# Optimization experiments

Measured on AMD Instinct MI355X. Metric: run time of the kernel, lower is better.

## Reference

```python
import jax, jax.numpy as jnp
import numpy as np

H = 32          # hidden_size
NUM_LAYERS = 3
B, T, IN = 16384, 64, 2


def _gru_dir(x, Wih, Whh, bih, bhh, reverse):
    """Single-direction GRU over x:[B,T,I] with PyTorch gate math."""
    # Precompute input projections for all timesteps: [B,T,3H]
    xg = jnp.einsum('bti,gi->btg', x, Wih) + bih
    if reverse:
        xg = xg[:, ::-1]

    def step(h, xt):
        gh = h @ Whh.T + bhh                      # [B,3H]
        xr, xz, xn = jnp.split(xt, 3, axis=-1)
        hr, hz, hn = jnp.split(gh, 3, axis=-1)
        r = jax.nn.sigmoid(xr + hr)
        z = jax.nn.sigmoid(xz + hz)
        n = jnp.tanh(xn + r * hn)
        h2 = (1.0 - z) * n + z * h
        return h2, h2

    h0 = jnp.zeros((x.shape[0], H), x.dtype)
    _, hs = jax.lax.scan(step, h0, jnp.swapaxes(xg, 0, 1))  # [T,B,H]
    hs = jnp.swapaxes(hs, 0, 1)                              # [B,T,H]
    if reverse:
        hs = hs[:, ::-1]
    return hs


def setup_inputs() -> dict:
    key = jax.random.key(0)
    ks = jax.random.split(key, 11)
    s = 0.2  # weight scale ~ uniform(-1/sqrt(H)) magnitude
    return {
        'x':    jax.random.normal(ks[0], (B, T, IN), jnp.float32),
        'Wih0': jax.random.normal(ks[1], (2, 3 * H, IN), jnp.float32) * s,
        'Whh0': jax.random.normal(ks[2], (2, 3 * H, H), jnp.float32) * s,
        'bih0': jax.random.normal(ks[3], (2, 3 * H), jnp.float32) * s,
        'bhh0': jax.random.normal(ks[4], (2, 3 * H), jnp.float32) * s,
        'Wih':  jax.random.normal(ks[5], (NUM_LAYERS - 1, 2, 3 * H, 2 * H), jnp.float32) * s,
        'Whh':  jax.random.normal(ks[6], (NUM_LAYERS - 1, 2, 3 * H, H), jnp.float32) * s,
        'bih':  jax.random.normal(ks[7], (NUM_LAYERS - 1, 2, 3 * H), jnp.float32) * s,
        'bhh':  jax.random.normal(ks[8], (NUM_LAYERS - 1, 2, 3 * H), jnp.float32) * s,
        'Wfc':  jax.random.normal(ks[9], (2, 2 * H), jnp.float32) * s,
        'bfc':  jax.random.normal(ks[10], (2,), jnp.float32) * s,
    }


def reference(x, Wih0, Whh0, bih0, bhh0, Wih, Whh, bih, bhh, Wfc, bfc):
    out = x
    for l in range(NUM_LAYERS):
        if l == 0:
            wi, wh, bi, bh = Wih0, Whh0, bih0, bhh0
        else:
            wi, wh, bi, bh = Wih[l - 1], Whh[l - 1], bih[l - 1], bhh[l - 1]
        fwd = _gru_dir(out, wi[0], wh[0], bi[0], bh[0], reverse=False)
        bwd = _gru_dir(out, wi[1], wh[1], bi[1], bh[1], reverse=True)
        out = jnp.concatenate([fwd, bwd], axis=-1)  # [B,T,2H]
    y = out @ Wfc.T + bfc                            # [B,T,2]
    return jnp.tanh(y)
```

## Files before the change

kernel.cpp:

```cpp
#include <hip/hip_runtime.h>
#include <cstdint>
#include <cstddef>


#define BB 16384
#define TT 64
#define ST ((size_t)BB * 64)
#define PT ((size_t)TT * BB * 2)

typedef __attribute__((ext_vector_type(8))) _Float16 f16x8;
typedef __attribute__((ext_vector_type(4))) float f32x4;

#if __has_builtin(__builtin_amdgcn_exp2f)
#define EXP2(x) __builtin_amdgcn_exp2f(x)
#else
#define EXP2(x) exp2f(x)
#endif
#if __has_builtin(__builtin_amdgcn_rcpf)
#define RCP(x) __builtin_amdgcn_rcpf(x)
#else
#define RCP(x) (1.0f / (x))
#endif

#define SR (-1.4426950408889634f)
#define SN (-2.8853900817779268f)

__device__ __forceinline__ float tanh_fast(float x) { return 2.0f / (1.0f + __expf(-2.0f * x)) - 1.0f; }
__device__ __forceinline__ unsigned short f2h(float f) {
    _Float16 h = (_Float16)f;
    return __builtin_bit_cast(unsigned short, h);
}
__device__ __forceinline__ unsigned int cvt_pkh(float a, float b) {
#if __has_builtin(__builtin_amdgcn_cvt_pkrtz)
    typedef __fp16 h2_t __attribute__((ext_vector_type(2)));
    h2_t p = __builtin_amdgcn_cvt_pkrtz(a, b);
    return __builtin_bit_cast(unsigned int, p);
#else
    return (unsigned int)f2h(a) | ((unsigned int)f2h(b) << 16);
#endif
}
__device__ __forceinline__ f32x4 mfma16h(f16x8 a, f16x8 b, f32x4 c) {
    return __builtin_amdgcn_mfma_f32_16x16x32_f16(a, b, c, 0, 0, 0);
}

__device__ __forceinline__ void gate_pair(float aR0, float aR1, float aZ0, float aZ1,
                                          float xN0, float xN1, float hN0, float hN1,
                                          float& hp0, float& hp1) {
    float er0 = EXP2(aR0), er1 = EXP2(aR1);
    float ez0 = EXP2(aZ0), ez1 = EXP2(aZ1);
    float Ar0 = 1.f + er0, Ar1 = 1.f + er1;
    float Az0 = 1.f + ez0, Az1 = 1.f + ez1;
    float iR = RCP(Ar0 * Ar1);
    float iZ = RCP(Az0 * Az1);
    float r0 = iR * Ar1, r1 = iR * Ar0;
    float z0 = iZ * Az1, z1 = iZ * Az0;
    float v0 = fmaf(r0, hN0, xN0), v1 = fmaf(r1, hN1, xN1);
    float en0 = EXP2(v0), en1 = EXP2(v1);
    float An0 = 1.f + en0, An1 = 1.f + en1;
    float iN = RCP(An0 * An1);
    float n0 = fmaf(2.f, iN * An1, -1.f);
    float n1 = fmaf(2.f, iN * An0, -1.f);
    hp0 = fmaf(z0, hp0 - n0, n0);
    hp1 = fmaf(z1, hp1 - n1, n1);
}


template<bool IS_L0, bool IS_LAST>
__global__ __launch_bounds__(256, 2)
void gru_mfma(const float* __restrict__ x0,
              const unsigned short* __restrict__ bin,
              const float* __restrict__ Wih,
              const float* __restrict__ Whh,
              const float* __restrict__ bih,
              const float* __restrict__ bhh,
              unsigned short* __restrict__ bout,
              const float* __restrict__ Wfc,
              float* __restrict__ pbase)
{
    const int tid  = threadIdx.x;
    const int lane = tid & 63;
    const int wv   = tid >> 6;
    const int g    = blockIdx.x * 4 + wv;
    const int d    = g >> 10;
    const int b0   = (g & 1023) * 16;
    const int col  = lane & 15;
    const int qd   = lane >> 4;

    f16x8 whhF[6];
    {
        const float* wsrc = Whh + d * 96 * 32;
        #pragma unroll
        for (int t = 0; t < 6; ++t) {
            const float sc = (t < 4) ? SR : SN;
            const int row = (t >> 1) * 32 + 8 * (col >> 2) + 4 * (t & 1) + (col & 3);
            const float* pr = wsrc + row * 32 + qd * 8;
            unsigned short wbits[8];
            #pragma unroll
            for (int j = 0; j < 8; ++j) wbits[j] = f2h(pr[j] * sc);
            whhF[t] = __builtin_bit_cast(f16x8, *(uint4*)wbits);
        }
    }

    f16x8 wihF[6][2];
    float w0c[6][4], w1c[6][4];
    if constexpr (!IS_L0) {
        const float* wsrc = Wih + d * 96 * 64;
        #pragma unroll
        for (int t = 0; t < 6; ++t) {
            const float sc = (t < 4) ? SR : SN;
            const int row = (t >> 1) * 32 + 8 * (col >> 2) + 4 * (t & 1) + (col & 3);
            #pragma unroll
            for (int kc = 0; kc < 2; ++kc) {
                const float* pr = wsrc + row * 64 + kc * 32 + qd * 8;
                unsigned short wbits[8];
                #pragma unroll
                for (int j = 0; j < 8; ++j) wbits[j] = f2h(pr[j] * sc);
                wihF[t][kc] = __builtin_bit_cast(f16x8, *(uint4*)wbits);
            }
        }
    } else {
        #pragma unroll
        for (int t = 0; t < 6; ++t) {
            const float sc = (t < 4) ? SR : SN;
            #pragma unroll
            for (int q = 0; q < 4; ++q) {
                const int row = (t >> 1) * 32 + 8 * qd + 4 * (t & 1) + q;
                const float* pr = Wih + d * 96 * 2 + row * 2;
                w0c[t][q] = pr[0] * sc;
                w1c[t][q] = pr[1] * sc;
            }
        }
    }

    f32x4 biasIn[6], biasHN[2];
    {
        const float* bi = bih + d * 96;
        const float* bh = bhh + d * 96;
        #pragma unroll
        for (int t = 0; t < 4; ++t) {
            const int off = (t >> 1) * 32 + 8 * qd + 4 * (t & 1);
            float4 a = *(const float4*)(bi + off);
            float4 b = *(const float4*)(bh + off);
            biasIn[t][0] = (a.x + b.x) * SR; biasIn[t][1] = (a.y + b.y) * SR;
            biasIn[t][2] = (a.z + b.z) * SR; biasIn[t][3] = (a.w + b.w) * SR;
        }
        #pragma unroll
        for (int T = 0; T < 2; ++T) {
            const int off = 64 + 8 * qd + 4 * T;
            float4 a = *(const float4*)(bi + off);
            float4 b = *(const float4*)(bh + off);
            biasIn[4 + T][0] = a.x * SN; biasIn[4 + T][1] = a.y * SN;
            biasIn[4 + T][2] = a.z * SN; biasIn[4 + T][3] = a.w * SN;
            biasHN[T][0] = b.x * SN; biasHN[T][1] = b.y * SN;
            biasHN[T][2] = b.z * SN; biasHN[T][3] = b.w * SN;
        }
    }

    float wf0[2][4], wf1[2][4];
    if constexpr (IS_LAST) {
        #pragma unroll
        for (int T = 0; T < 2; ++T)
            #pragma unroll
            for (int q = 0; q < 4; ++q) {
                const int u = 8 * qd + 4 * T + q;
                wf0[T][q] = Wfc[d * 32 + u];
                wf1[T][q] = Wfc[64 + d * 32 + u];
            }
    }

    const int t0 = d ? (TT - 1) : 0;
    const int dt = d ? -1 : 1;
    const ptrdiff_t dplane = (ptrdiff_t)dt * (ptrdiff_t)ST;

    f16x8 hF = {};
    float hprev[2][4] = {{0.f,0.f,0.f,0.f},{0.f,0.f,0.f,0.f}};

    auto REC = [&](f32x4 (&acc)[6], f32x4 (&accHN)[2]) {
        #pragma unroll
        for (int t = 0; t < 4; ++t)
            acc[t] = mfma16h(whhF[t], hF, acc[t]);
        #pragma unroll
        for (int T = 0; T < 2; ++T)
            accHN[T] = mfma16h(whhF[4 + T], hF, biasHN[T]);
    };

    auto PROJ = [&](f32x4 (&accN)[6], uint4 nx0, uint4 nx1, float2 nxs) {
        if constexpr (!IS_L0) {
            f16x8 a0 = __builtin_bit_cast(f16x8, nx0);
            f16x8 a1 = __builtin_bit_cast(f16x8, nx1);
            #pragma unroll
            for (int t = 0; t < 6; ++t) {
                accN[t] = mfma16h(wihF[t][0], a0, biasIn[t]);
                accN[t] = mfma16h(wihF[t][1], a1, accN[t]);
            }
        } else {
            #pragma unroll
            for (int t = 0; t < 6; ++t)
                #pragma unroll
                for (int q = 0; q < 4; ++q)
                    accN[t][q] = fmaf(nxs.x, w0c[t][q], fmaf(nxs.y, w1c[t][q], biasIn[t][q]));
        }
    };

    auto GATES = [&](f32x4 (&acc)[6], f32x4 (&accHN)[2], unsigned short* outp,
                     uint4& hwP, unsigned short*& opP, float* poutp) {
        unsigned int hw[4];
        #pragma unroll
        for (int T = 0; T < 2; ++T) {
            float h0 = hprev[T][0], h1 = hprev[T][1];
            float h2 = hprev[T][2], h3 = hprev[T][3];
            gate_pair(acc[T][0], acc[T][1], acc[2 + T][0], acc[2 + T][1],
                      acc[4 + T][0], acc[4 + T][1], accHN[T][0], accHN[T][1], h0, h1);
            gate_pair(acc[T][2], acc[T][3], acc[2 + T][2], acc[2 + T][3],
                      acc[4 + T][2], acc[4 + T][3], accHN[T][2], accHN[T][3], h2, h3);
            hprev[T][0] = h0; hprev[T][1] = h1; hprev[T][2] = h2; hprev[T][3] = h3;
            hw[2 * T]     = cvt_pkh(h0, h1);
            hw[2 * T + 1] = cvt_pkh(h2, h3);
        }
        hF = __builtin_bit_cast(f16x8, *(uint4*)hw);
        if constexpr (IS_LAST) {
            float p0 = 0.f, p1 = 0.f;
            #pragma unroll
            for (int T = 0; T < 2; ++T)
                #pragma unroll
                for (int q = 0; q < 4; ++q) {
                    p0 = fmaf(hprev[T][q], wf0[T][q], p0);
                    p1 = fmaf(hprev[T][q], wf1[T][q], p1);
                }
            p0 += __shfl_xor(p0, 16); p0 += __shfl_xor(p0, 32);
            p1 += __shfl_xor(p1, 16); p1 += __shfl_xor(p1, 32);
            if (qd == 0) *(float2*)poutp = make_float2(p0, p1);
        } else {
            *(uint4*)opP = hwP;
            hwP = *(uint4*)hw;
            opP = outp;
        }
    };

    f32x4 accA[6], accB[6], accHN[2];
    uint4 xc0 = {}, xc1 = {}, xe0 = {}, xe1 = {};
    float2 xsc = {}, xse = {};
    const unsigned short* xptrE = nullptr; const unsigned short* xptrO = nullptr;
    const float* xfpE = nullptr; const float* xfpO = nullptr;

    if constexpr (!IS_L0) {
        const unsigned short* p0 = bin + (size_t)t0 * ST + (size_t)(b0 + col) * 64 + qd * 8;
        uint4 a = *(const uint4*)p0, b = *(const uint4*)(p0 + 32);
        PROJ(accA, a, b, {});
        const unsigned short* p1 = p0 + dplane;
        xc0 = *(const uint4*)p1; xc1 = *(const uint4*)(p1 + 32);
        xptrE = p0 + 2 * dplane;
        xptrO = p0 + 3 * dplane;
    } else {
        const float* p0 = x0 + ((size_t)(b0 + col) * TT + t0) * 2;
        float2 xs0 = *(const float2*)p0;
        PROJ(accA, {}, {}, xs0);
        xsc = *(const float2*)(p0 + dt * 2);
        xfpE = p0 + dt * 4;
        xfpO = p0 + dt * 6;
    }

    unsigned short* optrA = nullptr; unsigned short* optrB = nullptr;
    float* poutA = nullptr; float* poutB = nullptr;
    const ptrdiff_t dpp = (ptrdiff_t)dt * (ptrdiff_t)BB * 2;
    if constexpr (IS_LAST) {
        poutA = pbase + (size_t)d * PT + ((size_t)t0 * BB + b0 + col) * 2;
        poutB = poutA + dpp;
    } else {
        optrA = bout + (size_t)t0 * ST + (size_t)(b0 + col) * 64 + d * 32 + qd * 8;
        optrB = optrA + dplane;
    }

    uint4 hwPrevA = {}, hwPrevB = {};
    unsigned short* opPrevA = optrA;
    unsigned short* opPrevB = optrB;

    for (int k = 0; k < 31; ++k) {
        if constexpr (!IS_L0) {
            xe0 = *(const uint4*)xptrE; xe1 = *(const uint4*)(xptrE + 32);
            xptrE += 2 * dplane;
        } else { xse = *(const float2*)xfpE; xfpE += dt * 4; }
        REC(accA, accHN);
        PROJ(accB, xc0, xc1, xsc);
        GATES(accA, accHN, optrA, hwPrevA, opPrevA, poutA);
        if constexpr (IS_LAST) poutA += 2 * dpp; else optrA += 2 * dplane;
        if constexpr (!IS_L0) {
            xc0 = *(const uint4*)xptrO; xc1 = *(const uint4*)(xptrO + 32);
            xptrO += 2 * dplane;
        } else { xsc = *(const float2*)xfpO; xfpO += dt * 4; }
        REC(accB, accHN);
        PROJ(accA, xe0, xe1, xse);
        GATES(accB, accHN, optrB, hwPrevB, opPrevB, poutB);
        if constexpr (IS_LAST) poutB += 2 * dpp; else optrB += 2 * dplane;
    }
    REC(accA, accHN);
    PROJ(accB, xc0, xc1, xsc);
    GATES(accA, accHN, optrA, hwPrevA, opPrevA, poutA);
    REC(accB, accHN);
    GATES(accB, accHN, optrB, hwPrevB, opPrevB, poutB);
    if constexpr (!IS_LAST) {
        *(uint4*)opPrevA = hwPrevA;
        *(uint4*)opPrevB = hwPrevB;
    }
}

__global__ __launch_bounds__(256)
void fc_finish(const float* __restrict__ pf,
               const float* __restrict__ pb,
               const float* __restrict__ bfc,
               float* __restrict__ out)
{
    __shared__ float2 tile[64][65];
    const int tid = threadIdx.x;
    const int bbase = blockIdx.x * 64;
    const float c0 = bfc[0], c1 = bfc[1];
    #pragma unroll
    for (int tp = 0; tp < 16; ++tp) {
        const int t = tp * 4 + (tid >> 6);
        const int bl = tid & 63;
        const size_t idx = ((size_t)t * BB + bbase + bl) * 2;
        float2 vf = *(const float2*)(pf + idx);
        float2 vb = *(const float2*)(pb + idx);
        float2 o;
        o.x = tanh_fast(vf.x + vb.x + c0);
        o.y = tanh_fast(vf.y + vb.y + c1);
        tile[t][bl] = o;
    }
    __syncthreads();
    #pragma unroll
    for (int bp = 0; bp < 16; ++bp) {
        const int bl = bp * 4 + (tid >> 6);
        const int t = tid & 63;
        *(float2*)(out + ((size_t)(bbase + bl) * TT + t) * 2) = tile[t][bl];
    }
}

extern "C" void kernel_launch(void* const* d_in, const int* in_sizes, int n_in,
                              void* d_out, int out_size, void* d_ws, size_t ws_size,
                              hipStream_t stream)
{
    const float* x    = (const float*)d_in[0];
    const float* Wih0 = (const float*)d_in[1];
    const float* Whh0 = (const float*)d_in[2];
    const float* bih0 = (const float*)d_in[3];
    const float* bhh0 = (const float*)d_in[4];
    const float* WihL = (const float*)d_in[5];
    const float* WhhL = (const float*)d_in[6];
    const float* bihL = (const float*)d_in[7];
    const float* bhhL = (const float*)d_in[8];
    const float* Wfc  = (const float*)d_in[9];
    const float* bfc  = (const float*)d_in[10];

    unsigned short* buf0 = (unsigned short*)d_ws;
    unsigned short* buf1 = buf0 + (size_t)TT * BB * 64;
    float* pbase = (float*)d_ws;
    float* out = (float*)d_out;

    gru_mfma<true, false><<<512, 256, 0, stream>>>(
        x, nullptr, Wih0, Whh0, bih0, bhh0, buf0, nullptr, nullptr);
    gru_mfma<false, false><<<512, 256, 0, stream>>>(
        nullptr, buf0, WihL, WhhL, bihL, bhhL, buf1, nullptr, nullptr);
    gru_mfma<false, true><<<512, 256, 0, stream>>>(
        nullptr, buf1, WihL + 2 * 96 * 64, WhhL + 2 * 96 * 32,
        bihL + 2 * 96, bhhL + 2 * 96, nullptr, Wfc, pbase);
    fc_finish<<<BB / 64, 256, 0, stream>>>(
        pbase, pbase + PT, bfc, out);
}
```

Before: 304.3 us.

## Split each GRU sequence tile across two waves exchanging hidden state via LDS

Each 16-sequence tile is now handled by a pair of wavefronts, each owning half the hidden units (one T half), instead of a single wave doing all 32 units. Per-step hidden halves are exchanged through shared memory with a block-wide barrier, and the FC partial sums are combined via LDS too. This doubles wave-level parallelism (1024 blocks) and halves per-wave MFMA/gate work on the serial recurrence path, at the cost of a __syncthreads every timestep and duplicated input loads.

```diff
diff --git a/kernel.cpp b/kernel.cpp
--- a/kernel.cpp
+++ b/kernel.cpp
@@ -77,95 +77,95 @@
               const float* __restrict__ Wfc,
               float* __restrict__ pbase)
 {
+    __shared__ uint2 hx[2][2][2][64];
+    __shared__ float2 fcx[2][2][16];
+
     const int tid  = threadIdx.x;
     const int lane = tid & 63;
     const int wv   = tid >> 6;
-    const int g    = blockIdx.x * 4 + wv;
-    const int d    = g >> 10;
-    const int b0   = (g & 1023) * 16;
+    const int pr   = wv >> 1;
+    const int Tw   = wv & 1;
+    const int g2   = blockIdx.x * 2 + pr;
+    const int d    = g2 >> 10;
+    const int b0   = (g2 & 1023) * 16;
     const int col  = lane & 15;
     const int qd   = lane >> 4;
 
-    f16x8 whhF[6];
+    f16x8 whhF[3];
     {
         const float* wsrc = Whh + d * 96 * 32;
         #pragma unroll
-        for (int t = 0; t < 6; ++t) {
-            const float sc = (t < 4) ? SR : SN;
-            const int row = (t >> 1) * 32 + 8 * (col >> 2) + 4 * (t & 1) + (col & 3);
-            const float* pr = wsrc + row * 32 + qd * 8;
+        for (int i = 0; i < 3; ++i) {
+            const float sc = (i < 2) ? SR : SN;
+            const int row = i * 32 + 8 * (col >> 2) + 4 * Tw + (col & 3);
+            const float* pr2 = wsrc + row * 32 + qd * 8;
             unsigned short wbits[8];
             #pragma unroll
-            for (int j = 0; j < 8; ++j) wbits[j] = f2h(pr[j] * sc);
-            whhF[t] = __builtin_bit_cast(f16x8, *(uint4*)wbits);
-        }
-    }
-
-    f16x8 wihF[6][2];
-    float w0c[6][4], w1c[6][4];
+            for (int j = 0; j < 8; ++j) wbits[j] = f2h(pr2[j] * sc);
+            whhF[i] = __builtin_bit_cast(f16x8, *(uint4*)wbits);
+        }
+    }
+
+    f16x8 wihF[3][2];
+    float w0c[3][4], w1c[3][4];
     if constexpr (!IS_L0) {
         const float* wsrc = Wih + d * 96 * 64;
         #pragma unroll
-        for (int t = 0; t < 6; ++t) {
-            const float sc = (t < 4) ? SR : SN;
-            const int row = (t >> 1) * 32 + 8 * (col >> 2) + 4 * (t & 1) + (col & 3);
+        for (int i = 0; i < 3; ++i) {
+            const float sc = (i < 2) ? SR : SN;
+            const int row = i * 32 + 8 * (col >> 2) + 4 * Tw + (col & 3);
             #pragma unroll
             for (int kc = 0; kc < 2; ++kc) {
-                const float* pr = wsrc + row * 64 + kc * 32 + qd * 8;
+                const float* pr2 = wsrc + row * 64 + kc * 32 + qd * 8;
                 unsigned short wbits[8];
                 #pragma unroll
-                for (int j = 0; j < 8; ++j) wbits[j] = f2h(pr[j] * sc);
-                wihF[t][kc] = __builtin_bit_cast(f16x8, *(uint4*)wbits);
+                for (int j = 0; j < 8; ++j) wbits[j] = f2h(pr2[j] * sc);
+                wihF[i][kc] = __builtin_bit_cast(f16x8, *(uint4*)wbits);
             }
         }
     } else {
         #pragma unroll
-        for (int t = 0; t < 6; ++t) {
-            const float sc = (t < 4) ? SR : SN;
+        for (int i = 0; i < 3; ++i) {
+            const float sc = (i < 2) ? SR : SN;
             #pragma unroll
             for (int q = 0; q < 4; ++q) {
-                const int row = (t >> 1) * 32 + 8 * qd + 4 * (t & 1) + q;
-                const float* pr = Wih + d * 96 * 2 + row * 2;
-                w0c[t][q] = pr[0] * sc;
-                w1c[t][q] = pr[1] * sc;
-            }
-        }
-    }
-
-    f32x4 biasIn[6], biasHN[2];
+                const int row = i * 32 + 8 * qd + 4 * Tw + q;
+                const float* pr2 = Wih + d * 96 * 2 + row * 2;
+                w0c[i][q] = pr2[0] * sc;
+                w1c[i][q] = pr2[1] * sc;
+            }
+        }
+    }
+
+    f32x4 biasIn[3], biasHN;
     {
         const float* bi = bih + d * 96;
         const float* bh = bhh + d * 96;
         #pragma unroll
-        for (int t = 0; t < 4; ++t) {
-            const int off = (t >> 1) * 32 + 8 * qd + 4 * (t & 1);
+        for (int i = 0; i < 2; ++i) {
+            const int off = i * 32 + 8 * qd + 4 * Tw;
             float4 a = *(const float4*)(bi + off);
             float4 b = *(const float4*)(bh + off);
-            biasIn[t][0] = (a.x + b.x) * SR; biasIn[t][1] = (a.y + b.y) * SR;
-            biasIn[t][2] = (a.z + b.z) * SR; biasIn[t][3] = (a.w + b.w) * SR;
-        }
-        #pragma unroll
-        for (int T = 0; T < 2; ++T) {
-            const int off = 64 + 8 * qd + 4 * T;
-            float4 a = *(const float4*)(bi + off);
-            float4 b = *(const float4*)(bh + off);
-            biasIn[4 + T][0] = a.x * SN; biasIn[4 + T][1] = a.y * SN;
-            biasIn[4 + T][2] = a.z * SN; biasIn[4 + T][3] = a.w * SN;
-            biasHN[T][0] = b.x * SN; biasHN[T][1] = b.y * SN;
-            biasHN[T][2] = b.z * SN; biasHN[T][3] = b.w * SN;
-        }
-    }
-
-    float wf0[2][4], wf1[2][4];
+            biasIn[i][0] = (a.x + b.x) * SR; biasIn[i][1] = (a.y + b.y) * SR;
+            biasIn[i][2] = (a.z + b.z) * SR; biasIn[i][3] = (a.w + b.w) * SR;
+        }
+        const int off = 64 + 8 * qd + 4 * Tw;
+        float4 a = *(const float4*)(bi + off);
+        float4 b = *(const float4*)(bh + off);
+        biasIn[2][0] = a.x * SN; biasIn[2][1] = a.y * SN;
+        biasIn[2][2] = a.z * SN; biasIn[2][3] = a.w * SN;
+        biasHN[0] = b.x * SN; biasHN[1] = b.y * SN;
+        biasHN[2] = b.z * SN; biasHN[3] = b.w * SN;
+    }
+
+    float wf0[4], wf1[4];
     if constexpr (IS_LAST) {
         #pragma unroll
-        for (int T = 0; T < 2; ++T)
-            #pragma unroll
-            for (int q = 0; q < 4; ++q) {
-                const int u = 8 * qd + 4 * T + q;
-                wf0[T][q] = Wfc[d * 32 + u];
-                wf1[T][q] = Wfc[64 + d * 32 + u];
-            }
+        for (int q = 0; q < 4; ++q) {
+            const int u = 8 * qd + 4 * Tw + q;
+            wf0[q] = Wfc[d * 32 + u];
+            wf1[q] = Wfc[64 + d * 32 + u];
+        }
     }
 
     const int t0 = d ? (TT - 1) : 0;
@@ -173,71 +173,81 @@
     const ptrdiff_t dplane = (ptrdiff_t)dt * (ptrdiff_t)ST;
 
     f16x8 hF = {};
-    float hprev[2][4] = {{0.f,0.f,0.f,0.f},{0.f,0.f,0.f,0.f}};
-
-    auto REC = [&](f32x4 (&acc)[6], f32x4 (&accHN)[2]) {
-        #pragma unroll
-        for (int t = 0; t < 4; ++t)
-            acc[t] = mfma16h(whhF[t], hF, acc[t]);
-        #pragma unroll
-        for (int T = 0; T < 2; ++T)
-            accHN[T] = mfma16h(whhF[4 + T], hF, biasHN[T]);
+    float hprev[4] = {0.f, 0.f, 0.f, 0.f};
+
+    uint2* hxwA = &hx[0][pr][Tw][lane];
+    const uint2* hxrA = &hx[0][pr][Tw ^ 1][lane];
+    uint2* hxwB = &hx[1][pr][Tw][lane];
+    const uint2* hxrB = &hx[1][pr][Tw ^ 1][lane];
+    float2* fcw = &fcx[pr][Tw][0];
+    const float2* fcr = &fcx[pr][Tw ^ 1][0];
+
+    auto REC = [&](f32x4 (&acc)[3], f32x4& accHN) {
+        acc[0] = mfma16h(whhF[0], hF, acc[0]);
+        acc[1] = mfma16h(whhF[1], hF, acc[1]);
+        accHN  = mfma16h(whhF[2], hF, biasHN);
     };
 
-    auto PROJ = [&](f32x4 (&accN)[6], uint4 nx0, uint4 nx1, float2 nxs) {
+    auto PROJ = [&](f32x4 (&accN)[3], uint4 nx0, uint4 nx1, float2 nxs) {
         if constexpr (!IS_L0) {
             f16x8 a0 = __builtin_bit_cast(f16x8, nx0);
             f16x8 a1 = __builtin_bit_cast(f16x8, nx1);
             #pragma unroll
-            for (int t = 0; t < 6; ++t) {
-                accN[t] = mfma16h(wihF[t][0], a0, biasIn[t]);
-                accN[t] = mfma16h(wihF[t][1], a1, accN[t]);
+            for (int i = 0; i < 3; ++i) {
+                accN[i] = mfma16h(wihF[i][0], a0, biasIn[i]);
+                accN[i] = mfma16h(wihF[i][1], a1, accN[i]);
             }
         } else {
             #pragma unroll
-            for (int t = 0; t < 6; ++t)
+            for (int i = 0; i < 3; ++i)
                 #pragma unroll
                 for (int q = 0; q < 4; ++q)
-                    accN[t][q] = fmaf(nxs.x, w0c[t][q], fmaf(nxs.y, w1c[t][q], biasIn[t][q]));
+                    accN[i][q] = fmaf(nxs.x, w0c[i][q], fmaf(nxs.y, w1c[i][q], biasIn[i][q]));
         }
     };
 
-    auto GATES = [&](f32x4 (&acc)[6], f32x4 (&accHN)[2], unsigned short* outp,
+    auto GATES = [&](f32x4 (&acc)[3], f32x4& accHN, unsigned short* outp,
+                     uint2* hxw, const uint2* hxr,
                      uint4& hwP, unsigned short*& opP, float* poutp) {
-        unsigned int hw[4];
-        #pragma unroll
-        for (int T = 0; T < 2; ++T) {
-            float h0 = hprev[T][0], h1 = hprev[T][1];
-            float h2 = hprev[T][2], h3 = hprev[T][3];
-            gate_pair(acc[T][0], acc[T][1], acc[2 + T][0], acc[2 + T][1],
-                      acc[4 + T][0], acc[4 + T][1], accHN[T][0], accHN[T][1], h0, h1);
-            gate_pair(acc[T][2], acc[T][3], acc[2 + T][2], acc[2 + T][3],
-                      acc[4 + T][2], acc[4 + T][3], accHN[T][2], accHN[T][3], h2, h3);
-            hprev[T][0] = h0; hprev[T][1] = h1; hprev[T][2] = h2; hprev[T][3] = h3;
-            hw[2 * T]     = cvt_pkh(h0, h1);
-            hw[2 * T + 1] = cvt_pkh(h2, h3);
-        }
-        hF = __builtin_bit_cast(f16x8, *(uint4*)hw);
+        float h0 = hprev[0], h1 = hprev[1], h2 = hprev[2], h3 = hprev[3];
+        gate_pair(acc[0][0], acc[0][1], acc[1][0], acc[1][1],
+                  acc[2][0], acc[2][1], accHN[0], accHN[1], h0, h1);
+        gate_pair(acc[0][2], acc[0][3], acc[1][2], acc[1][3],
+                  acc[2][2], acc[2][3], accHN[2], accHN[3], h2, h3);
+        hprev[0] = h0; hprev[1] = h1; hprev[2] = h2; hprev[3] = h3;
+        uint2 own = make_uint2(cvt_pkh(h0, h1), cvt_pkh(h2, h3));
+        *hxw = own;
+        float p0 = 0.f, p1 = 0.f;
         if constexpr (IS_LAST) {
-            float p0 = 0.f, p1 = 0.f;
-            #pragma unroll
-            for (int T = 0; T < 2; ++T)
-                #pragma unroll
-                for (int q = 0; q < 4; ++q) {
-                    p0 = fmaf(hprev[T][q], wf0[T][q], p0);
-                    p1 = fmaf(hprev[T][q], wf1[T][q], p1);
-                }
+            #pragma unroll
+            for (int q = 0; q < 4; ++q) {
+                p0 = fmaf(hprev[q], wf0[q], p0);
+                p1 = fmaf(hprev[q], wf1[q], p1);
+            }
             p0 += __shfl_xor(p0, 16); p0 += __shfl_xor(p0, 32);
             p1 += __shfl_xor(p1, 16); p1 += __shfl_xor(p1, 32);
-            if (qd == 0) *(float2*)poutp = make_float2(p0, p1);
+            if (qd == 0) fcw[col] = make_float2(p0, p1);
+        }
+        __syncthreads();
+        uint2 oth = *hxr;
+        uint4 comb = (Tw == 0) ? make_uint4(own.x, own.y, oth.x, oth.y)
+                               : make_uint4(oth.x, oth.y, own.x, own.y);
+        hF = __builtin_bit_cast(f16x8, comb);
+        if constexpr (IS_LAST) {
+            if (Tw == 0 && qd == 0) {
+                float2 o2 = fcr[col];
+                *(float2*)poutp = make_float2(p0 + o2.x, p1 + o2.y);
+            }
         } else {
-            *(uint4*)opP = hwP;
-            hwP = *(uint4*)hw;
-            opP = outp;
+            if (Tw == 0) {
+                *(uint4*)opP = hwP;
+                hwP = comb;
+                opP = outp;
+            }
         }
     };
 
-    f32x4 accA[6], accB[6], accHN[2];
+    f32x4 accA[3], accB[3], accHN;
     uint4 xc0 = {}, xc1 = {}, xe0 = {}, xe1 = {};
     float2 xsc = {}, xse = {};
     const unsigned short* xptrE = nullptr; const unsigned short* xptrO = nullptr;
@@ -282,7 +292,7 @@
         } else { xse = *(const float2*)xfpE; xfpE += dt * 4; }
         REC(accA, accHN);
         PROJ(accB, xc0, xc1, xsc);
-        GATES(accA, accHN, optrA, hwPrevA, opPrevA, poutA);
+        GATES(accA, accHN, optrA, hxwA, hxrA, hwPrevA, opPrevA, poutA);
         if constexpr (IS_LAST) poutA += 2 * dpp; else optrA += 2 * dplane;
         if constexpr (!IS_L0) {
             xc0 = *(const uint4*)xptrO; xc1 = *(const uint4*)(xptrO + 32);
@@ -290,17 +300,19 @@
         } else { xsc = *(const float2*)xfpO; xfpO += dt * 4; }
         REC(accB, accHN);
         PROJ(accA, xe0, xe1, xse);
-        GATES(accB, accHN, optrB, hwPrevB, opPrevB, poutB);
+        GATES(accB, accHN, optrB, hxwB, hxrB, hwPrevB, opPrevB, poutB);
         if constexpr (IS_LAST) poutB += 2 * dpp; else optrB += 2 * dplane;
     }
     REC(accA, accHN);
     PROJ(accB, xc0, xc1, xsc);
-    GATES(accA, accHN, optrA, hwPrevA, opPrevA, poutA);
+    GATES(accA, accHN, optrA, hxwA, hxrA, hwPrevA, opPrevA, poutA);
     REC(accB, accHN);
-    GATES(accB, accHN, optrB, hwPrevB, opPrevB, poutB);
+    GATES(accB, accHN, optrB, hxwB, hxrB, hwPrevB, opPrevB, poutB);
     if constexpr (!IS_LAST) {
-        *(uint4*)opPrevA = hwPrevA;
-        *(uint4*)opPrevB = hwPrevB;
+        if (Tw == 0) {
+            *(uint4*)opPrevA = hwPrevA;
+            *(uint4*)opPrevB = hwPrevB;
+        }
     }
 }
 
@@ -356,11 +368,11 @@
     float* pbase = (float*)d_ws;
     float* out = (float*)d_out;
 
-    gru_mfma<true, false><<<512, 256, 0, stream>>>(
+    gru_mfma<true, false><<<1024, 256, 0, stream>>>(
         x, nullptr, Wih0, Whh0, bih0, bhh0, buf0, nullptr, nullptr);
-    gru_mfma<false, false><<<512, 256, 0, stream>>>(
+    gru_mfma<false, false><<<1024, 256, 0, stream>>>(
         nullptr, buf0, WihL, WhhL, bihL, bhhL, buf1, nullptr, nullptr);
-    gru_mfma<false, true><<<512, 256, 0, stream>>>(
+    gru_mfma<false, true><<<1024, 256, 0, stream>>>(
         nullptr, buf1, WihL + 2 * 96 * 64, WhhL + 2 * 96 * 32,
         bihL + 2 * 96, bhhL + 2 * 96, nullptr, Wfc, pbase);
     fc_finish<<<BB / 64, 256, 0, stream>>>(
```

Result: slower. 352.3 us (+15.8%).
